# Kernel tuning notes

Measured on AMD Instinct MI355X. Metric: run time of the kernel, lower is better.

## Reference

```python
import jax, jax.numpy as jnp
import numpy as np

EPS = 0.1  # label smoothing

def lstm_scan(x, Wih, Whh, b, reverse=False):
    # x: [B,T,D] -> outputs [B,T,H]; PyTorch gate order i,f,g,o; zero initial state
    B = x.shape[0]; H = Whh.shape[1]
    def cell(carry, xt):
        h, c = carry
        g = xt @ Wih.T + h @ Whh.T + b
        i, f, gg, o = jnp.split(g, 4, axis=-1)
        c2 = jax.nn.sigmoid(f) * c + jax.nn.sigmoid(i) * jnp.tanh(gg)
        h2 = jax.nn.sigmoid(o) * jnp.tanh(c2)
        return (h2, c2), h2
    init = (jnp.zeros((B, H), x.dtype), jnp.zeros((B, H), x.dtype))
    _, hs = jax.lax.scan(cell, init, jnp.swapaxes(x, 0, 1), reverse=reverse)
    return jnp.swapaxes(hs, 0, 1)

def _forward(x, x_mask, y, y_mask,
             enc_l1_Wih, enc_l1_Whh, enc_l1_b, enc_l2_Wih, enc_l2_Whh, enc_l2_b,
             enc_l3_Wih, enc_l3_Whh, enc_l3_b, blstm_f_Wih, blstm_f_Whh, blstm_f_b,
             blstm_b_Wih, blstm_b_Whh, blstm_b_b, conv1_W, conv1_b, conv2_W, conv2_b,
             emb, att_Wih, att_Whh, att_b, w_W, w_b, v_W, v_b, w_att_v,
             dec_Wih, dec_Whh, dec_b, cls_W, cls_b):
    B, T, F0 = x.shape
    pad = (-T) % 4
    # mod_pad + mod_cat: stack 4 consecutive frames -> [B, T//4, 4*F0]
    xp = jnp.pad(x, ((0, 0), (0, pad), (0, 0)))
    xs = xp.reshape(B, (T + pad) // 4, 4 * F0)
    mp = jnp.pad(x_mask, ((0, 0), (0, pad), (0, 0)))
    m = mp[:, ::4, :]  # [B, T', 1]
    # ---- Encoder ----
    h = lstm_scan(xs, enc_l1_Wih, enc_l1_Whh, enc_l1_b)
    h = lstm_scan(h, enc_l2_Wih, enc_l2_Whh, enc_l2_b)
    h = lstm_scan(h, enc_l3_Wih, enc_l3_Whh, enc_l3_b) * m
    bf = lstm_scan(h, blstm_f_Wih, blstm_f_Whh, blstm_f_b)
    bb = lstm_scan(h, blstm_b_Wih, blstm_b_Whh, blstm_b_b, reverse=True)
    bl = jnp.concatenate([bf, bb], axis=-1) * m  # [B,T',1024]
    c1 = jax.nn.leaky_relu(bl @ conv1_W.T + conv1_b, negative_slope=0.1)  # dropout = eval identity
    eout = (c1 @ conv2_W.T + conv2_b) * m  # [B,T',256]
    # ---- Decoder (attention loop via scan) ----
    att_h = eout @ w_W.T + w_b  # [B,T',256]
    embed = emb[y[:, :-1]]      # [B,L-1,256]
    mask_add = (m[:, :, 0] - 1.0) * 1e30  # [B,T']
    P = att_Whh.shape[1]
    h0 = jnp.zeros((B, P), eout.dtype)
    carry0 = (h0, h0, jnp.zeros((B, P), eout.dtype))
    def step(carry, e_t):
        hh, cc, ctx = carry
        body = jnp.concatenate([e_t, ctx], axis=-1)
        g = body @ att_Wih.T + hh @ att_Whh.T + att_b
        i, f, gg, o = jnp.split(g, 4, axis=-1)
        cc = jax.nn.sigmoid(f) * cc + jax.nn.sigmoid(i) * jnp.tanh(gg)
        hh = jax.nn.sigmoid(o) * jnp.tanh(cc)
        state = hh @ v_W.T + v_b  # [B,256]
        score = jnp.sum(w_att_v * jnp.tanh(state[:, None, :] + att_h), axis=-1) + mask_add
        alpha = jax.nn.softmax(score, axis=1)  # [B,T']
        ctx = jnp.sum(eout * alpha[:, :, None], axis=1)  # [B,256]
        return (hh, cc, ctx), (hh, ctx)
    _, (lstms, ctxs) = jax.lax.scan(step, carry0, jnp.swapaxes(embed, 0, 1))
    lstms = jnp.swapaxes(lstms, 0, 1)  # [B,L-1,256]
    ctxs = jnp.swapaxes(ctxs, 0, 1)
    ym = y_mask[:, 1:, None]
    att_fea = jnp.concatenate([lstms * ym, ctxs * ym], axis=-1)  # [B,L-1,512]
    dout = lstm_scan(att_fea, dec_Wih, dec_Whh, dec_b)
    dout = jnp.concatenate([att_fea, dout], axis=-1) * ym  # [B,L-1,768]; dropout = eval identity
    logit = dout @ cls_W.T + cls_b  # [B,L-1,V]
    # ---- Label smoothing CE over real tokens ----
    V = cls_b.shape[0]
    logp = jax.nn.log_softmax(logit, axis=-1)
    label = y[:, 1:]
    mask = (y_mask[:, 1:] > 0).astype(logit.dtype)
    n = jnp.sum(mask)
    smooth = jnp.sum(-jnp.sum(logp, axis=-1) * mask) / n
    nll = jnp.sum(-jnp.take_along_axis(logp, label[:, :, None], axis=-1)[:, :, 0] * mask) / n
    return smooth * EPS / V + (1.0 - EPS) * nll

def setup_inputs() -> dict:
    B, T, F0, L, V = 32, 4096, 80, 65, 4235
    H, P = 512, 256
    key = jax.random.key(0)
    ks = iter(jax.random.split(key, 64))
    def rn(shape, s=0.05):
        return (jax.random.normal(next(ks), shape, jnp.float32) * s)
    inp = {}
    inp['x'] = jax.random.normal(next(ks), (B, T, F0), jnp.float32)
    inp['x_mask'] = jnp.ones((B, T, 1), jnp.float32)
    inp['y'] = jax.random.randint(next(ks), (B, L), 0, V)
    inp['y_mask'] = jnp.ones((B, L), jnp.float32)
    Din = 4 * F0
    inp['enc_l1_Wih'] = rn((4 * H, Din)); inp['enc_l1_Whh'] = rn((4 * H, H)); inp['enc_l1_b'] = jnp.zeros((4 * H,), jnp.float32)
    inp['enc_l2_Wih'] = rn((4 * H, H)); inp['enc_l2_Whh'] = rn((4 * H, H)); inp['enc_l2_b'] = jnp.zeros((4 * H,), jnp.float32)
    inp['enc_l3_Wih'] = rn((4 * H, H)); inp['enc_l3_Whh'] = rn((4 * H, H)); inp['enc_l3_b'] = jnp.zeros((4 * H,), jnp.float32)
    inp['blstm_f_Wih'] = rn((4 * H, H)); inp['blstm_f_Whh'] = rn((4 * H, H)); inp['blstm_f_b'] = jnp.zeros((4 * H,), jnp.float32)
    inp['blstm_b_Wih'] = rn((4 * H, H)); inp['blstm_b_Whh'] = rn((4 * H, H)); inp['blstm_b_b'] = jnp.zeros((4 * H,), jnp.float32)
    inp['conv1_W'] = rn((H, 2 * H)); inp['conv1_b'] = jnp.zeros((H,), jnp.float32)
    inp['conv2_W'] = rn((P, H)); inp['conv2_b'] = jnp.zeros((P,), jnp.float32)
    inp['emb'] = rn((V, P), 1.0)
    inp['att_Wih'] = rn((4 * P, 2 * P)); inp['att_Whh'] = rn((4 * P, P)); inp['att_b'] = jnp.zeros((4 * P,), jnp.float32)
    inp['w_W'] = rn((P, P)); inp['w_b'] = jnp.zeros((P,), jnp.float32)
    inp['v_W'] = rn((P, P)); inp['v_b'] = jnp.zeros((P,), jnp.float32)
    inp['w_att_v'] = rn((P,))
    inp['dec_Wih'] = rn((4 * P, 2 * P)); inp['dec_Whh'] = rn((4 * P, P)); inp['dec_b'] = jnp.zeros((4 * P,), jnp.float32)
    inp['cls_W'] = rn((V, 3 * P)); inp['cls_b'] = jnp.zeros((V,), jnp.float32)
    return inp

def reference(x, x_mask, y, y_mask, enc_l1_Wih, enc_l1_Whh, enc_l1_b, enc_l2_Wih, enc_l2_Whh, enc_l2_b, enc_l3_Wih, enc_l3_Whh, enc_l3_b, blstm_f_Wih, blstm_f_Whh, blstm_f_b, blstm_b_Wih, blstm_b_Whh, blstm_b_b, conv1_W, conv1_b, conv2_W, conv2_b, emb, att_Wih, att_Whh, att_b, w_W, w_b, v_W, v_b, w_att_v, dec_Wih, dec_Whh, dec_b, cls_W, cls_b):
    return _forward(x, x_mask, y, y_mask, enc_l1_Wih, enc_l1_Whh, enc_l1_b, enc_l2_Wih, enc_l2_Whh, enc_l2_b, enc_l3_Wih, enc_l3_Whh, enc_l3_b, blstm_f_Wih, blstm_f_Whh, blstm_f_b, blstm_b_Wih, blstm_b_Whh, blstm_b_b, conv1_W, conv1_b, conv2_W, conv2_b, emb, att_Wih, att_Whh, att_b, w_W, w_b, v_W, v_b, w_att_v, dec_Wih, dec_Whh, dec_b, cls_W, cls_b)
```

## Files before the change

kernel.cpp:

```cpp
#include <hip/hip_runtime.h>
#include <math.h>

#define DEV static __device__ __forceinline__
typedef unsigned short u16;
typedef unsigned int u32;

typedef __attribute__((ext_vector_type(8))) __bf16 bf16x8;
typedef __attribute__((ext_vector_type(4))) float f32x4;

DEV float sigm(float x){ return 1.0f/(1.0f+__expf(-x)); }
DEV float tanh_f(float x){ float e=__expf(2.0f*x); return 1.0f - 2.0f/(e+1.0f); }

DEV float b2f(u16 u){ union {u32 i; float f;} c; c.i = ((u32)u)<<16; return c.f; }
DEV u16 f2b(float f){ union {u32 i; float f;} c; c.f = f; u32 r = (c.i + 0x7FFFu + ((c.i>>16)&1u)) >> 16; return (u16)r; }

DEV void cstore(u32* p, u32 v){ __hip_atomic_store(p, v, __ATOMIC_RELAXED, __HIP_MEMORY_SCOPE_SYSTEM); }
DEV u32  cload(const u32* p){ return __hip_atomic_load(p, __ATOMIC_RELAXED, __HIP_MEMORY_SCOPE_SYSTEM); }

#define FSTRIDE 32
DEV void waitflags(unsigned* flags, unsigned target, int nwg){
  const int lane = threadIdx.x & 63;
  unsigned long long spin = 0;
  for(;;){
    bool ok = true;
    for (int j=lane; j<nwg; j+=64)
      ok &= ((int)(cload(&flags[j*FSTRIDE]) - target) >= 0);
    if (__all(ok)) break;
    if (++spin > 2000000ull) break;
    __builtin_amdgcn_s_sleep(1);
  }
}

struct PL2 { const float *Wih, *Whh, *bias; const u16* xplain; u16* hout; int kx, maskout; };
struct PA2 {
  PL2 L[4];
  u16* ex;
  u16* exm;
  const float* xm;
  unsigned* flags;
  int T, nwg, rev; unsigned base;
};

#define VWAIT(N) { asm volatile("s_waitcnt vmcnt(" #N ")" ::: "memory"); __builtin_amdgcn_sched_barrier(0); }

#define STAGE_LO(LL, Q, TT) { \
  const char* base_; int coh_; \
  if ((LL)==0){ base_=(const char*)A.L[0].xplain + ((long)(TT)*32768) + w*512; coh_=0; } \
  else if (NL==4 && (LL)==3){ base_=(const char*)A.exm + (long)par*32768 + w*512; coh_=1; } \
  else { base_=(const char*)A.ex + (long)(((LL)-1)*2+par)*32768 + w*512; coh_=1; } \
  _Pragma("unroll") \
  for (int i_=0;i_<8;++i_){ \
    int rl_=i_*2+(lane>>5); \
    int b_=bh*16+rl_; \
    const char* src_=base_ + (long)b_*1024 + (((lane&31)*16) ^ ((rl_&7)<<4)); \
    char* dst_=Vs + (Q)*32768 + w*8192 + i_*1024 + lane*16; \
    if (coh_) __builtin_amdgcn_global_load_lds((const u32*)src_,(u32*)dst_,16,0,0x11); \
    else      __builtin_amdgcn_global_load_lds((const u32*)src_,(u32*)dst_,16,0,0); \
  } }

#define STAGE_HI(LL, Q) { \
  const char* base_=(const char*)A.ex + (long)((LL)*2+par)*32768 + (w-2)*512; \
  _Pragma("unroll") \
  for (int i_=0;i_<8;++i_){ \
    int rl_=i_*2+(lane>>5); \
    int b_=bh*16+rl_; \
    const char* src_=base_ + (long)b_*1024 + (((lane&31)*16) ^ ((rl_&7)<<4)); \
    char* dst_=Vs + (Q)*32768 + w*8192 + i_*1024 + lane*16; \
    __builtin_amdgcn_global_load_lds((const u32*)src_,(u32*)dst_,16,0,0x11); \
  } }

#define STAGE_ALL(LL, Q, TT) { if (w<2) STAGE_LO(LL, Q, TT) else STAGE_HI(LL, Q) }

#define DOMFMA(LL, Q) { \
  const char* vb_=Vs + (Q)*32768 + w*8192; \
  const int sw_=(cl&7)<<4; \
  f32x4 a0_={0.f,0.f,0.f,0.f}, a1_={0.f,0.f,0.f,0.f}; \
  _Pragma("unroll") \
  for (int f_=0;f_<8;++f_){ \
    union{ bf16x8 v; uint4 q; } aa_; \
    aa_.q = *(const uint4*)(vb_ + cl*512 + ((f_*64+lg*16) ^ sw_)); \
    a0_=__builtin_amdgcn_mfma_f32_16x16x32_bf16(aa_.v, bw[LL][0][f_], a0_,0,0,0); \
    a1_=__builtin_amdgcn_mfma_f32_16x16x32_bf16(aa_.v, bw[LL][1][f_], a1_,0,0,0); \
  } \
  *(f32x4*)&P[(LL)*2560 + (w*32 + cl)*20 + lg*4] = a0_; \
  *(f32x4*)&P[(LL)*2560 + (w*32 + 16 + cl)*20 + lg*4] = a1_; \
  __builtin_amdgcn_sched_barrier(0); }

template<int NL>
__global__ __launch_bounds__(256,1) void pipe2(PA2 A){
  __shared__ __align__(16) char Vs[98304];
  __shared__ float P[NL*2560];
  const int t = threadIdx.x, wg = blockIdx.x;
  const int bh = wg>>6, cg = wg&63;
  const int w = t>>6, lane = t&63;
  const int cl = lane&15, lg = lane>>4;
  u32* exu  = (u32*)A.ex;
  u32* exmu = (u32*)A.exm;
  bf16x8 bw[NL][2][8];
  #pragma unroll
  for (int l=0;l<NL;++l){
    const int kx = A.L[l].kx;
    #pragma unroll
    for (int nt=0; nt<2; ++nt){
      const int c32 = nt*16 + cl;
      const int r = (c32&3)*512 + cg*8 + (c32>>2);
      #pragma unroll
      for (int f=0;f<8;++f){
        union { bf16x8 v; u16 s[8]; } u;
        int k8 = w*256 + f*32 + lg*8;
        if (k8 < 512){
          if (k8 < kx){
            const float* p = A.L[l].Wih + (long)r*kx + k8;
            for (int j=0;j<8;++j) u.s[j]=f2b(p[j]);
          } else { for (int j=0;j<8;++j) u.s[j]=0; }
        } else {
          const float* p = A.L[l].Whh + (long)r*512 + (k8-512);
          for (int j=0;j<8;++j) u.s[j]=f2b(p[j]);
        }
        bw[l][nt][f]=u.v;
      }
    }
  }
  float bias_r[NL][4];
  float cst_r[NL];
  #pragma unroll
  for (int l=0;l<NL;++l) cst_r[l]=0.f;
  if (t<128){
    const int uu = t>>4;
    #pragma unroll
    for (int l=0;l<NL;++l)
      #pragma unroll
      for (int g=0;g<4;++g)
        bias_r[l][g] = A.L[l].bias[g*512 + cg*8 + uu];
  }
  {
    const int tot = (NL==4)? 640 : 128;
    for (int i=t;i<tot;i+=256){
      int l5=i>>7, rem=i&127;
      int par0=rem>>6, bl=(rem>>2)&15, j=rem&3;
      int b=bh*16+bl;
      u32* p = (l5<NL)? exu + (l5*2+par0)*8192 + b*256 + cg*4 + j
                      : exmu + par0*8192 + b*256 + cg*4 + j;
      cstore(p,0);
    }
  }
  __syncthreads();
  if (t==0) cstore(&A.flags[wg*FSTRIDE], A.base+1);
  const int T = A.T;
  unsigned* myflags = A.flags + (bh*64)*FSTRIDE;
  for (int s=0; s<T+NL-1; ++s){
    const int par = (s-1)&1;
    if constexpr (NL==1){
      const int tt0 = A.rev ? (T-1-s) : s;
      if (w<2) STAGE_LO(0,0,tt0)
      waitflags(myflags, A.base+s+1, 64);
      if (w>=2) STAGE_HI(0,0)
      VWAIT(0)
      DOMFMA(0,0)
    } else {
      if (s>=3 && s<=T-1){
        const int tt0 = A.rev ? (T-1-s) : s;
        if (w<2) STAGE_LO(0,0,tt0)
        waitflags(myflags, A.base+s+1, 64);
        if (w>=2) STAGE_HI(0,0)
        STAGE_ALL(1,1,0)
        STAGE_ALL(2,2,0)
        VWAIT(16) DOMFMA(0,0)
        asm volatile("s_waitcnt lgkmcnt(0)" ::: "memory");
        __builtin_amdgcn_sched_barrier(0);
        STAGE_ALL(3,0,0)
        VWAIT(16) DOMFMA(1,1)
        VWAIT(8)  DOMFMA(2,2)
        VWAIT(0)  DOMFMA(3,0)
      } else {
        waitflags(myflags, A.base+s+1, 64);
        #pragma unroll
        for (int l=0;l<NL;++l){
          const int sc = s-l;
          if (sc<0 || sc>=T) continue;
          const int ttl = A.rev ? (T-1-sc) : sc;
          STAGE_ALL(l, (l&1), ttl)
          VWAIT(0)
          DOMFMA(l, (l&1))
        }
      }
    }
    __syncthreads();
    if (t<128){
      const int bl = t&15, uu = t>>4;
      const int b = bh*16 + bl;
      #pragma unroll
      for (int l=0;l<NL;++l){
        const int sc = s-l;
        if (sc<0 || sc>=T) continue;
        const int tt = A.rev ? (T-1-sc) : sc;
        float g4[4];
        #pragma unroll
        for (int g=0;g<4;++g){
          const int c32 = uu*4+g;
          float sum = bias_r[l][g];
          #pragma unroll
          for (int ww=0;ww<4;++ww) sum += P[l*2560 + (ww*32+c32)*20 + bl];
          g4[g]=sum;
        }
        float c2 = sigm(g4[1])*cst_r[l] + sigm(g4[0])*tanh_f(g4[2]);
        float h2 = sigm(g4[3])*tanh_f(c2);
        cst_r[l]=c2;
        float h2n = __shfl_down(h2, 16);
        if (!(uu&1)){
          u32 pk = (u32)f2b(h2) | ((u32)f2b(h2n)<<16);
          cstore(exu + (l*2+(s&1))*8192 + b*256 + cg*4 + (uu>>1), pk);
        }
        if (NL==4 && l==2){
          float m = A.xm[b*4096 + 4*tt];
          float hm = h2*m;
          float hmn = __shfl_down(hm, 16);
          if (!(uu&1)){
            u32 pk = (u32)f2b(hm) | ((u32)f2b(hmn)<<16);
            cstore(exmu + (s&1)*8192 + b*256 + cg*4 + (uu>>1), pk);
          }
          if (A.L[2].hout) A.L[2].hout[((long)tt*32+b)*512 + cg*8+uu] = f2b(hm);
        } else if (A.L[l].hout){
          float ov = h2;
          if (A.L[l].maskout) ov *= A.xm[b*4096 + 4*tt];
          A.L[l].hout[((long)tt*32+b)*512 + cg*8+uu] = f2b(ov);
        }
      }
    }
    __syncthreads();
    if (t==0) cstore(&A.flags[wg*FSTRIDE], A.base+s+2);
  }
}

__global__ __launch_bounds__(256,1) void dec_rec2(
    const u16* __restrict__ xin, const float* __restrict__ Wih,
    const float* __restrict__ Whh, const float* __restrict__ bias,
    float* __restrict__ dout, u16* __restrict__ exd,
    unsigned* flags, unsigned base, int T)
{
  __shared__ __align__(16) char Vs[49152];
  __shared__ float P[2304];
  __shared__ float cst[128];
  __shared__ float biasl[16];
  const int t = threadIdx.x, wg = blockIdx.x;
  const int u0 = wg*4;
  const int w = t>>6, lane = t&63, c = lane&15, lg = lane>>4;
  const int r = (c&3)*256 + u0 + (c>>2);
  u32* exu = (u32*)exd;
  const int nf = (w<2) ? 8 : 4;
  bf16x8 bw[8];
  #pragma unroll
  for (int f=0;f<8;++f){
    union { bf16x8 v; u16 s[8]; } u;
    if (f < nf){
      if (w<2){
        const float* p = Wih + (long)r*512 + w*256 + f*32 + lg*8;
        for (int j=0;j<8;++j) u.s[j]=f2b(p[j]);
      } else {
        const float* p = Whh + (long)r*256 + (w-2)*128 + f*32 + lg*8;
        for (int j=0;j<8;++j) u.s[j]=f2b(p[j]);
      }
    } else { for (int j=0;j<8;++j) u.s[j]=0; }
    bw[f]=u.v;
  }
  if (t<16) biasl[t] = bias[(t&3)*256 + u0 + (t>>2)];
  if (t<128) cst[t]=0.f;
  if (t<128){
    int par=(t>>6)&1, b=(t>>1)&31, j=t&1;
    cstore(exu + par*4096 + b*128 + wg*2 + j, 0);
  }
  __syncthreads();
  if (t==0) cstore(&flags[wg*FSTRIDE], base+1);
  const int waveOff = (w<2) ? w*16384 : 32768 + (w-2)*8192;
  const int NI  = (w<2) ? 16 : 8;
  const int rpi = (w<2) ? 2 : 4;
  const int sb  = (w<2) ? (lane>>5) : (lane>>4);
  const int coffb = (w<2) ? (lane&31)*16 : (lane&15)*16;
  const int rowB = (w<2) ? 512 : 256;
  for (int s=0; s<T; ++s){
    if (w<2){
      #pragma unroll
      for (int i=0;i<16;++i){
        int b = i*rpi + sb;
        const char* src = (const char*)xin + (long)s*32768 + w*512 + b*1024 + (coffb ^ ((b&7)<<4));
        void* ldst = (void*)(Vs + waveOff + i*1024);
        __builtin_amdgcn_global_load_lds((const u32*)src, (u32*)ldst, 16, 0, 0);
      }
    }
    waitflags(flags, base+s+1, 64);
    const int par = (s-1)&1;
    if (w>=2){
      #pragma unroll
      for (int i=0;i<8;++i){
        int b = i*rpi + sb;
        const char* src = (const char*)exd + par*16384 + (w-2)*256 + b*512 + (coffb ^ ((b&7)<<4));
        void* ldst = (void*)(Vs + waveOff + i*1024);
        __builtin_amdgcn_global_load_lds((const u32*)src, (u32*)ldst, 16, 0, 0x11);
      }
    }
    asm volatile("s_waitcnt vmcnt(0)" ::: "memory");
    __builtin_amdgcn_sched_barrier(0);
    f32x4 acc0={0.f,0.f,0.f,0.f}, acc1={0.f,0.f,0.f,0.f};
    const int b1 = c+16;
    #pragma unroll
    for (int f=0;f<8;++f){
      if (f>=nf) break;
      int koff = f*64 + lg*16;
      union { bf16x8 v; uint4 q; } a0, a1;
      a0.q = *(const uint4*)(Vs + waveOff + c *rowB + (koff ^ ((c &7)<<4)));
      a1.q = *(const uint4*)(Vs + waveOff + b1*rowB + (koff ^ ((b1&7)<<4)));
      acc0 = __builtin_amdgcn_mfma_f32_16x16x32_bf16(a0.v, bw[f], acc0, 0,0,0);
      acc1 = __builtin_amdgcn_mfma_f32_16x16x32_bf16(a1.v, bw[f], acc1, 0,0,0);
    }
    {
      float* pp = &P[(w*16+c)*36 + lg*4];
      *(f32x4*)pp      = acc0;
      *(f32x4*)(pp+16) = acc1;
    }
    __syncthreads();
    if (t<128){
      const int b = t&31, uu = t>>5, wpw = t>>6;
      float g4[4];
      #pragma unroll
      for (int g=0; g<4; ++g){
        int cc = uu*4+g;
        float sum = biasl[cc];
        #pragma unroll
        for (int ww=0; ww<4; ++ww) sum += P[(ww*16+cc)*36 + b];
        g4[g]=sum;
      }
      float c2 = sigm(g4[1])*cst[t] + sigm(g4[0])*tanh_f(g4[2]);
      float h2 = sigm(g4[3])*tanh_f(c2);
      cst[t]=c2;
      u32 hv = (u32)f2b(h2);
      u32 ot = (u32)__shfl_xor((int)hv, 32);
      if (lane<32)
        cstore(exu + (s&1)*4096 + b*128 + wg*2 + wpw, (hv&0xffffu)|(ot<<16));
      dout[((long)s*32+b)*256 + u0+uu] = h2;
    }
    __syncthreads();
    if (t==0) cstore(&flags[wg*FSTRIDE], base+s+2);
  }
}

__global__ void cvt_x(const float* __restrict__ x, u16* __restrict__ xp){
  long id8 = ((long)blockIdx.x*256 + threadIdx.x)*8;
  int rr = (int)(id8 >> 9); int k = (int)(id8 & 511);
  int tt = rr >> 5, b = rr & 31;
  union { uint4 q; u16 s[8]; } u;
  if (k < 320){
    const float* p = x + (long)b*327680 + (long)tt*320 + k;
    float4 v0 = *(const float4*)p, v1 = *(const float4*)(p+4);
    u.s[0]=f2b(v0.x); u.s[1]=f2b(v0.y); u.s[2]=f2b(v0.z); u.s[3]=f2b(v0.w);
    u.s[4]=f2b(v1.x); u.s[5]=f2b(v1.y); u.s[6]=f2b(v1.z); u.s[7]=f2b(v1.w);
  } else {
    for (int j=0;j<8;++j) u.s[j]=0;
  }
  *(uint4*)(xp + id8) = u.q;
}

template<int ABF, int CBF>
__global__ __launch_bounds__(256,2) void gemm_mfma(
  const void* __restrict__ A0, long lda0, const void* __restrict__ A1, long lda1, int K0,
  const float* __restrict__ W, const float* __restrict__ bias, void* __restrict__ C,
  int M, int N, int K, int ldw, int act, const float* __restrict__ xmask)
{
  __shared__ __align__(16) u16 As[64*32];
  __shared__ __align__(16) u16 Bs[64*32];
  const int t = threadIdx.x;
  const int m0 = blockIdx.x*64, n0 = blockIdx.y*64;
  const int w = t>>6, lane = t&63;
  const int al = lane&15, lg = lane>>4;
  f32x4 acc[4];
  #pragma unroll
  for (int i=0;i<4;++i) acc[i] = (f32x4){0.f,0.f,0.f,0.f};
  const int srow = t>>2, kq = t&3;
  const int spos = (kq ^ (srow&3))*8;
  for (int k0=0; k0<K; k0+=32){
    {
      int kk = k0 + kq*8;
      const void* Ab; long lda; int kof;
      if (kk < K0){ Ab=A0; lda=lda0; kof=kk; } else { Ab=A1; lda=lda1; kof=kk-K0; }
      union { uint4 q; u16 s[8]; } u;
      if (ABF){
        u.q = *(const uint4*)((const u16*)Ab + (long)(m0+srow)*lda + kof);
      } else {
        const float* ap = (const float*)Ab + (long)(m0+srow)*lda + kof;
        float4 x0 = *(const float4*)ap, x1 = *(const float4*)(ap+4);
        u.s[0]=f2b(x0.x); u.s[1]=f2b(x0.y); u.s[2]=f2b(x0.z); u.s[3]=f2b(x0.w);
        u.s[4]=f2b(x1.x); u.s[5]=f2b(x1.y); u.s[6]=f2b(x1.z); u.s[7]=f2b(x1.w);
      }
      *(uint4*)&As[srow*32 + spos] = u.q;
    }
    {
      int n = n0 + srow;
      union { uint4 q; u16 s[8]; } u;
      if (n < N){
        const float* wp = W + (long)n*ldw + k0 + kq*8;
        float4 y0 = *(const float4*)wp, y1 = *(const float4*)(wp+4);
        u.s[0]=f2b(y0.x); u.s[1]=f2b(y0.y); u.s[2]=f2b(y0.z); u.s[3]=f2b(y0.w);
        u.s[4]=f2b(y1.x); u.s[5]=f2b(y1.y); u.s[6]=f2b(y1.z); u.s[7]=f2b(y1.w);
      } else {
        for (int j=0;j<8;++j) u.s[j]=0;
      }
      *(uint4*)&Bs[srow*32 + spos] = u.q;
    }
    __syncthreads();
    union { bf16x8 v; uint4 q; } a;
    a.q = *(const uint4*)&As[(w*16+al)*32 + ((lg ^ (al&3))*8)];
    #pragma unroll
    for (int nt=0; nt<4; ++nt){
      union { bf16x8 v; uint4 q; } b;
      b.q = *(const uint4*)&Bs[(nt*16+al)*32 + ((lg ^ (al&3))*8)];
      acc[nt] = __builtin_amdgcn_mfma_f32_16x16x32_bf16(a.v, b.v, acc[nt], 0,0,0);
    }
    __syncthreads();
  }
  #pragma unroll
  for (int nt=0; nt<4; ++nt){
    int n = n0 + nt*16 + al;
    if (n >= N) continue;
    float bv = bias[n];
    #pragma unroll
    for (int j=0;j<4;++j){
      int m = m0 + w*16 + lg*4 + j;
      float v = acc[nt][j] + bv;
      if (act) v = (v > 0.f) ? v : 0.1f*v;
      if (xmask) v *= xmask[(m&31)*4096 + 4*(m>>5)];
      if (CBF) ((u16*)C)[(long)m*N + n] = f2b(v);
      else     ((float*)C)[(long)m*N + n] = v;
    }
  }
}

__global__ void embed_gather(const float* __restrict__ emb, const int* __restrict__ y,
                             float* __restrict__ out){
  int id = blockIdx.x*256 + threadIdx.x;
  int p = id&255, r = id>>8;
  int l = r>>5, b = r&31;
  out[id] = emb[(long)y[b*65 + l]*256 + p];
}

__global__ void zero_f(float* __restrict__ p, int n){
  int id = blockIdx.x*256 + threadIdx.x;
  if (id < n) p[id] = 0.f;
}

__global__ void set_val(float* p, float v){ p[0] = v; }

__global__ void attfea_k(const float* __restrict__ lstms, const float* __restrict__ ctxs,
                         const float* __restrict__ ym, float* __restrict__ attf,
                         u16* __restrict__ attfb){
  long id4 = ((long)blockIdx.x*256 + threadIdx.x)*4;
  int r = (int)(id4>>9); int f = (int)(id4&511);
  int l = r>>5, b = r&31;
  float m = ym[b*65 + l + 1];
  float4 v = (f<256) ? *(const float4*)(lstms + (long)r*256 + f)
                     : *(const float4*)(ctxs  + (long)r*256 + (f-256));
  v.x*=m; v.y*=m; v.z*=m; v.w*=m;
  *(float4*)(attf + id4) = v;
  u16* ob = attfb + id4;
  ob[0]=f2b(v.x); ob[1]=f2b(v.y); ob[2]=f2b(v.z); ob[3]=f2b(v.w);
}

__global__ void dcat_k(const float* __restrict__ attf, const float* __restrict__ dout,
                       const float* __restrict__ ym, float* __restrict__ dcat){
  long id4 = ((long)blockIdx.x*256 + threadIdx.x)*4;
  int r = (int)(id4/768); int f = (int)(id4 - (long)r*768);
  int l = r>>5, b = r&31;
  float m = ym[b*65 + l + 1];
  float4 v = (f<512) ? *(const float4*)(attf + (long)r*512 + f)
                     : *(const float4*)(dout + (long)r*256 + (f-512));
  v.x*=m; v.y*=m; v.z*=m; v.w*=m;
  *(float4*)(dcat + id4) = v;
}

__global__ __launch_bounds__(256,1) void k1_dec(
  const float* __restrict__ bodyR, float* __restrict__ bodyW,
  const float* __restrict__ epart, const float* __restrict__ Whh,
  const float* __restrict__ Wih, float* __restrict__ cc,
  float* __restrict__ lstms, int s)
{
  __shared__ __align__(16) float vT[512*36];
  __shared__ float gl[32*32];
  const int t = threadIdx.x, wg = blockIdx.x;
  for (int i = t*4; i < 32*512; i += 1024){
    int b = i>>9, k = i&511;
    float4 v = *(const float4*)(bodyR + b*512 + k);
    vT[(k+0)*36+b]=v.x; vT[(k+1)*36+b]=v.y; vT[(k+2)*36+b]=v.z; vT[(k+3)*36+b]=v.w;
  }
  __syncthreads();
  const int c_l = t>>3, bq = t&7;
  const int col = (c_l&3)*256 + wg*8 + (c_l>>2);
  float a0=0.f,a1=0.f,a2=0.f,a3=0.f;
  for (int k=0;k<256;k+=4){
    float4 w = *(const float4*)(Whh + (long)col*256 + k);
    const float* vp = &vT[k*36 + bq*4];
    float4 v0=*(const float4*)(vp), v1=*(const float4*)(vp+36), v2=*(const float4*)(vp+72), v3=*(const float4*)(vp+108);
    a0 += w.x*v0.x + w.y*v1.x + w.z*v2.x + w.w*v3.x;
    a1 += w.x*v0.y + w.y*v1.y + w.z*v2.y + w.w*v3.y;
    a2 += w.x*v0.z + w.y*v1.z + w.z*v2.z + w.w*v3.z;
    a3 += w.x*v0.w + w.y*v1.w + w.z*v2.w + w.w*v3.w;
  }
  for (int k=256;k<512;k+=4){
    float4 w = *(const float4*)(Wih + (long)col*512 + k);
    const float* vp = &vT[k*36 + bq*4];
    float4 v0=*(const float4*)(vp), v1=*(const float4*)(vp+36), v2=*(const float4*)(vp+72), v3=*(const float4*)(vp+108);
    a0 += w.x*v0.x + w.y*v1.x + w.z*v2.x + w.w*v3.x;
    a1 += w.x*v0.y + w.y*v1.y + w.z*v2.y + w.w*v3.y;
    a2 += w.x*v0.z + w.y*v1.z + w.z*v2.z + w.w*v3.z;
    a3 += w.x*v0.w + w.y*v1.w + w.z*v2.w + w.w*v3.w;
  }
  gl[c_l*32+bq*4+0] = a0 + epart[((long)s*32 + bq*4+0)*1024 + col];
  gl[c_l*32+bq*4+1] = a1 + epart[((long)s*32 + bq*4+1)*1024 + col];
  gl[c_l*32+bq*4+2] = a2 + epart[((long)s*32 + bq*4+2)*1024 + col];
  gl[c_l*32+bq*4+3] = a3 + epart[((long)s*32 + bq*4+3)*1024 + col];
  __syncthreads();
  {
    const int u_ = t>>5, b = t&31, ug = wg*8 + u_;
    const float gi=gl[(u_*4+0)*32+b], gf=gl[(u_*4+1)*32+b], gg=gl[(u_*4+2)*32+b], go=gl[(u_*4+3)*32+b];
    float c0 = cc[b*256+ug];
    float c2 = sigm(gf)*c0 + sigm(gi)*tanh_f(gg);
    float h2 = sigm(go)*tanh_f(c2);
    cc[b*256+ug] = c2;
    bodyW[b*512 + ug] = h2;
    lstms[((long)s*32 + b)*256 + ug] = h2;
  }
}

__global__ __launch_bounds__(256,1) void k2_dec(
  const float* __restrict__ bodyW, const float* __restrict__ vW,
  const float* __restrict__ vb, float* __restrict__ state)
{
  __shared__ __align__(16) float hT[256*36];
  const int t = threadIdx.x, wg = blockIdx.x;
  for (int i = t*4; i < 8192; i += 1024){
    int b = i>>8, k = i&255;
    float4 v = *(const float4*)(bodyW + b*512 + k);
    hT[(k+0)*36+b]=v.x; hT[(k+1)*36+b]=v.y; hT[(k+2)*36+b]=v.z; hT[(k+3)*36+b]=v.w;
  }
  __syncthreads();
  const int p = wg*32 + (t>>3), bq = t&7;
  float a0=0.f,a1=0.f,a2=0.f,a3=0.f;
  for (int k=0;k<256;k+=4){
    float4 w = *(const float4*)(vW + (long)p*256 + k);
    const float* vp = &hT[k*36 + bq*4];
    float4 v0=*(const float4*)(vp), v1=*(const float4*)(vp+36), v2=*(const float4*)(vp+72), v3=*(const float4*)(vp+108);
    a0 += w.x*v0.x + w.y*v1.x + w.z*v2.x + w.w*v3.x;
    a1 += w.x*v0.y + w.y*v1.y + w.z*v2.y + w.w*v3.y;
    a2 += w.x*v0.z + w.y*v1.z + w.z*v2.z + w.w*v3.z;
    a3 += w.x*v0.w + w.y*v1.w + w.z*v2.w + w.w*v3.w;
  }
  float bb = vb[p];
  state[(bq*4+0)*256 + p] = a0 + bb;
  state[(bq*4+1)*256 + p] = a1 + bb;
  state[(bq*4+2)*256 + p] = a2 + bb;
  state[(bq*4+3)*256 + p] = a3 + bb;
}

__global__ __launch_bounds__(256,1) void k3_dec(
  const float* __restrict__ state, const u16* __restrict__ atth,
  const float* __restrict__ wav, const float* __restrict__ xm,
  float* __restrict__ sc, float* __restrict__ scm)
{
  __shared__ float st[256], wv[256], red[256];
  const int t = threadIdx.x;
  const int b = blockIdx.x>>2, ch = blockIdx.x&3;
  st[t] = state[b*256 + t];
  wv[t] = wav[t];
  __syncthreads();
  const int tp = ch*256 + t;
  const u16* ap = atth + ((long)tp*32 + b)*256;
  float acc = 0.f;
  for (int p=0;p<256;p+=4){
    ushort4 a = *(const ushort4*)(ap+p);
    acc += wv[p+0]*tanh_f(st[p+0]+b2f(a.x));
    acc += wv[p+1]*tanh_f(st[p+1]+b2f(a.y));
    acc += wv[p+2]*tanh_f(st[p+2]+b2f(a.z));
    acc += wv[p+3]*tanh_f(st[p+3]+b2f(a.w));
  }
  acc += (xm[b*4096 + 4*tp] - 1.0f)*1e30f;
  sc[b*1024 + tp] = acc;
  red[t] = acc;
  __syncthreads();
  for (int o=128;o>0;o>>=1){ if (t<o) red[t]=fmaxf(red[t],red[t+o]); __syncthreads(); }
  if (t==0) scm[b*4+ch] = red[0];
}

__global__ __launch_bounds__(256,1) void k4_dec(
  const float* __restrict__ sc, const float* __restrict__ scm,
  const u16* __restrict__ eout, float* __restrict__ ctxs,
  float* __restrict__ bodyW, int s)
{
  __shared__ float al[1024];
  __shared__ float red[256];
  const int t = threadIdx.x, b = blockIdx.x;
  float m = fmaxf(fmaxf(scm[b*4+0],scm[b*4+1]), fmaxf(scm[b*4+2],scm[b*4+3]));
  float ps = 0.f;
  #pragma unroll
  for (int j=0;j<4;++j){
    int tp = t + j*256;
    float e = __expf(sc[b*1024+tp] - m);
    al[tp] = e; ps += e;
  }
  red[t]=ps; __syncthreads();
  for (int o=128;o>0;o>>=1){ if (t<o) red[t]+=red[t+o]; __syncthreads(); }
  float rinv = 1.0f/red[0];
  float acc = 0.f;
  const u16* ep = eout + b*256 + t;
  for (int tp=0;tp<1024;++tp) acc += al[tp] * b2f(ep[(long)tp*8192]);
  float cv = acc*rinv;
  ctxs[((long)s*32 + b)*256 + t] = cv;
  bodyW[b*512 + 256 + t] = cv;
}

__global__ __launch_bounds__(256,1) void loss_row(
  const float* __restrict__ logits, const int* __restrict__ y,
  const float* __restrict__ ym, float* __restrict__ rows)
{
  __shared__ float red[256];
  const int r = blockIdx.x, t = threadIdx.x;
  const float* row = logits + (long)r*4235;
  float mx = -3.0e38f;
  for (int i=t;i<4235;i+=256) mx = fmaxf(mx, row[i]);
  red[t]=mx; __syncthreads();
  for (int o=128;o>0;o>>=1){ if (t<o) red[t]=fmaxf(red[t],red[t+o]); __syncthreads(); }
  const float M = red[0];
  __syncthreads();
  float se=0.f, sl=0.f;
  for (int i=t;i<4235;i+=256){ float v=row[i]; se += __expf(v-M); sl += v; }
  red[t]=se; __syncthreads();
  for (int o=128;o>0;o>>=1){ if (t<o) red[t]+=red[t+o]; __syncthreads(); }
  const float SE = red[0];
  __syncthreads();
  red[t]=sl; __syncthreads();
  for (int o=128;o>0;o>>=1){ if (t<o) red[t]+=red[t+o]; __syncthreads(); }
  const float SL = red[0];
  if (t==0){
    const int tt = r>>5, b = r&31;
    const float lse = M + logf(SE);
    const float mk = (ym[b*65 + tt + 1] > 0.f) ? 1.f : 0.f;
    rows[r]        = (4235.0f*lse - SL)*mk;
    rows[2048 + r] = (lse - row[y[b*65 + tt + 1]])*mk;
    rows[4096 + r] = mk;
  }
}

__global__ __launch_bounds__(256,1) void loss_final(const float* __restrict__ rows, float* __restrict__ out){
  __shared__ float red[256];
  const int t = threadIdx.x;
  float s1=0.f,s2=0.f,s3=0.f;
  for (int i=t;i<2048;i+=256){ s1+=rows[i]; s2+=rows[2048+i]; s3+=rows[4096+i]; }
  red[t]=s1; __syncthreads();
  for (int o=128;o>0;o>>=1){ if (t<o) red[t]+=red[t+o]; __syncthreads(); }
  const float S = red[0]; __syncthreads();
  red[t]=s2; __syncthreads();
  for (int o=128;o>0;o>>=1){ if (t<o) red[t]+=red[t+o]; __syncthreads(); }
  const float NL = red[0]; __syncthreads();
  red[t]=s3; __syncthreads();
  for (int o=128;o>0;o>>=1){ if (t<o) red[t]+=red[t+o]; __syncthreads(); }
  const float N = red[0];
  if (t==0){
    float n = (N > 0.f) ? N : 1.f;
    out[0] = (S/n)*(0.1f/4235.0f) + 0.9f*(NL/n);
  }
}

extern "C" void kernel_launch(void* const* d_in, const int* in_sizes, int n_in,
                              void* d_out, int out_size, void* d_ws, size_t ws_size,
                              hipStream_t stream)
{
  const float* x    = (const float*)d_in[0];
  const float* xm   = (const float*)d_in[1];
  const int*   y    = (const int*)  d_in[2];
  const float* ym   = (const float*)d_in[3];
  const float* l1_Wih=(const float*)d_in[4];  const float* l1_Whh=(const float*)d_in[5];  const float* l1_b=(const float*)d_in[6];
  const float* l2_Wih=(const float*)d_in[7];  const float* l2_Whh=(const float*)d_in[8];  const float* l2_b=(const float*)d_in[9];
  const float* l3_Wih=(const float*)d_in[10]; const float* l3_Whh=(const float*)d_in[11]; const float* l3_b=(const float*)d_in[12];
  const float* bf_Wih=(const float*)d_in[13]; const float* bf_Whh=(const float*)d_in[14]; const float* bf_b=(const float*)d_in[15];
  const float* bb_Wih=(const float*)d_in[16]; const float* bb_Whh=(const float*)d_in[17]; const float* bb_b=(const float*)d_in[18];
  const float* c1_W=(const float*)d_in[19]; const float* c1_b=(const float*)d_in[20];
  const float* c2_W=(const float*)d_in[21]; const float* c2_b=(const float*)d_in[22];
  const float* emb =(const float*)d_in[23];
  const float* att_Wih=(const float*)d_in[24]; const float* att_Whh=(const float*)d_in[25]; const float* att_b=(const float*)d_in[26];
  const float* w_W=(const float*)d_in[27]; const float* w_b=(const float*)d_in[28];
  const float* v_W=(const float*)d_in[29]; const float* v_b=(const float*)d_in[30];
  const float* wav=(const float*)d_in[31];
  const float* dec_Wih=(const float*)d_in[32]; const float* dec_Whh=(const float*)d_in[33]; const float* dec_b=(const float*)d_in[34];
  const float* cls_W=(const float*)d_in[35]; const float* cls_b=(const float*)d_in[36];

  const size_t REQ = 137625600ull;
  if (ws_size < REQ){
    set_val<<<1,1,0,stream>>>((float*)d_out, -(float)(ws_size>>20));
    return;
  }
  char* ws = (char*)d_ws;
  unsigned* FLAGS  = (unsigned*)(ws);
  unsigned* FLAGSD = (unsigned*)(ws + 16384);
  u16* EXU  = (u16*)(ws + 65536);
  u16* EXM  = (u16*)(ws + 327680);
  u16* EXD  = (u16*)(ws + 393216);
  u16* XP   = (u16*)(ws + 2097152);
  u16* HS2  = (u16*)(ws + 35651584);
  u16* HSF  = (u16*)(ws + 69206016);
  u16* HSB  = XP;
  u16* C1OUT = HS2;
  u16* EOUTB = HSF;
  u16* ATTHB = (u16*)(ws + 85983232);
  float* LOGIT = (float*)XP;
  float* AR    = (float*)(ws + 102760448);
  float* EMBED = AR;
  float* EPART = EMBED + 524288;
  float* LSTMS = EPART + 2097152;
  float* CTXS  = LSTMS + 524288;
  float* ATTF  = CTXS  + 524288;
  float* DOUT  = ATTF  + 1048576;
  float* DCAT  = DOUT  + 524288;
  float* SC    = DCAT  + 1572864;
  float* SCM   = SC    + 32768;
  float* ROWS  = SCM   + 128;
  float* BODY  = ROWS  + 6144;
  float* CC    = BODY  + 32768;
  float* STATE = CC    + 8192;
  u16*  ATTFB  = (u16*)(STATE + 8192);

  (void)hipMemsetAsync(ws, 0, 32768, stream);

  cvt_x<<<8192,256,0,stream>>>(x, XP);
  PA2 pa;
  pa.L[0] = { l1_Wih, l1_Whh, l1_b, XP,      nullptr, 320, 0 };
  pa.L[1] = { l2_Wih, l2_Whh, l2_b, nullptr, nullptr, 512, 0 };
  pa.L[2] = { l3_Wih, l3_Whh, l3_b, nullptr, HS2,     512, 0 };
  pa.L[3] = { bf_Wih, bf_Whh, bf_b, nullptr, HSF,     512, 1 };
  pa.ex = EXU; pa.exm = EXM; pa.xm = xm; pa.flags = FLAGS;
  pa.T = 1024; pa.nwg = 128; pa.rev = 0; pa.base = 0;
  pipe2<4><<<128,256,0,stream>>>(pa);
  PA2 pb;
  pb.L[0] = { bb_Wih, bb_Whh, bb_b, HS2, HSB, 512, 1 };
  pb.L[1] = pb.L[0]; pb.L[2] = pb.L[0]; pb.L[3] = pb.L[0];
  pb.ex = EXU; pb.exm = EXM; pb.xm = xm; pb.flags = FLAGS;
  pb.T = 1024; pb.nwg = 128; pb.rev = 1; pb.base = 1028;
  pipe2<1><<<128,256,0,stream>>>(pb);
  gemm_mfma<1,1><<<dim3(512,8),256,0,stream>>>(HSF, 512, HSB, 512, 512,
      c1_W, c1_b, C1OUT, 32768, 512, 1024, 1024, 1, nullptr);
  gemm_mfma<1,1><<<dim3(512,4),256,0,stream>>>(C1OUT, 512, C1OUT, 512, 512,
      c2_W, c2_b, EOUTB, 32768, 256, 512, 512, 0, xm);
  gemm_mfma<1,1><<<dim3(512,4),256,0,stream>>>(EOUTB, 256, EOUTB, 256, 256,
      w_W, w_b, ATTHB, 32768, 256, 256, 256, 0, nullptr);

  embed_gather<<<2048,256,0,stream>>>(emb, y, EMBED);
  gemm_mfma<0,0><<<dim3(32,16),256,0,stream>>>(EMBED, 256, EMBED, 256, 256,
      att_Wih, att_b, EPART, 2048, 1024, 256, 512, 0, nullptr);
  zero_f<<<160,256,0,stream>>>(BODY, 40960);
  for (int s=0;s<64;++s){
    float* bodyR = BODY + (s&1)*16384;
    float* bodyW = BODY + ((s+1)&1)*16384;
    k1_dec<<<32,256,0,stream>>>(bodyR, bodyW, EPART, att_Whh, att_Wih, CC, LSTMS, s);
    k2_dec<<<8,256,0,stream>>>(bodyW, v_W, v_b, STATE);
    k3_dec<<<128,256,0,stream>>>(STATE, ATTHB, wav, xm, SC, SCM);
    k4_dec<<<32,256,0,stream>>>(SC, SCM, EOUTB, CTXS, bodyW, s);
  }
  attfea_k<<<1024,256,0,stream>>>(LSTMS, CTXS, ym, ATTF, ATTFB);
  dec_rec2<<<64,256,0,stream>>>(ATTFB, dec_Wih, dec_Whh, dec_b,
      DOUT, EXD, FLAGSD, 0u, 64);
  dcat_k<<<1536,256,0,stream>>>(ATTF, DOUT, ym, DCAT);
  gemm_mfma<0,0><<<dim3(32,67),256,0,stream>>>(DCAT, 768, DCAT, 768, 768,
      cls_W, cls_b, LOGIT, 2048, 4235, 768, 768, 0, nullptr);
  loss_row<<<2048,256,0,stream>>>(LOGIT, y, ym, ROWS);
  loss_final<<<1,256,0,stream>>>(ROWS, (float*)d_out);
}
```

Before: 18.23 ms.

## Fuse attention decoder loop into one persistent kernel with flag barriers

Replaces the 256 small per-step kernel launches of the attention decoder (k1..k4 for each of 64 steps) with a single persistent 128-workgroup kernel. Grid-wide spin-flag barriers separate the LSTM, state-projection/score and softmax-context phases. The v_W projection is now computed redundantly per workgroup instead of in a separate kernel. This removes launch overhead and inter-kernel gaps, but adds system-scope atomic loads/stores, spin-wait cost, and reliance on all 128 workgroups being co-resident.

```diff
diff --git a/kernel.cpp b/kernel.cpp
--- a/kernel.cpp
+++ b/kernel.cpp
@@ -16,6 +16,8 @@
 
 DEV void cstore(u32* p, u32 v){ __hip_atomic_store(p, v, __ATOMIC_RELAXED, __HIP_MEMORY_SCOPE_SYSTEM); }
 DEV u32  cload(const u32* p){ return __hip_atomic_load(p, __ATOMIC_RELAXED, __HIP_MEMORY_SCOPE_SYSTEM); }
+DEV float cloadf(const float* p){ union{u32 i;float f;}c; c.i = cload((const u32*)p); return c.f; }
+DEV void cstoref(float* p, float v){ union{u32 i;float f;}c; c.f = v; cstore((u32*)p, c.i); }
 
 #define FSTRIDE 32
 DEV void waitflags(unsigned* flags, unsigned target, int nwg){
@@ -343,6 +345,144 @@
   }
 }
 
+__global__ __launch_bounds__(256,1) void dec_att(
+  const float* __restrict__ epart, const float* __restrict__ Whh,
+  const float* __restrict__ Wih, const float* __restrict__ vW,
+  const float* __restrict__ vb, const float* __restrict__ wav,
+  const u16* __restrict__ atth, const u16* __restrict__ eout,
+  const float* __restrict__ xm,
+  float* __restrict__ body, float* __restrict__ cc,
+  float* __restrict__ lstms, float* __restrict__ ctxs,
+  float* __restrict__ sc, float* __restrict__ scm,
+  unsigned* __restrict__ flags)
+{
+  __shared__ __align__(16) char LDSB[77824];
+  const int t = threadIdx.x, wg = blockIdx.x;
+  if (wg < 64) cstoref(body + wg*256 + t, 0.f);
+  if (wg < 32) cc[((t&31))*256 + wg*8 + (t>>5)] = 0.f;
+  __syncthreads();
+  if (t==0) cstore(&flags[wg*FSTRIDE], 1);
+  waitflags(flags, 1, 128);
+  for (int s=0; s<64; ++s){
+    float* bodyR = body + (s&1)*16384;
+    float* bodyW = body + ((s+1)&1)*16384;
+    if (wg < 32){
+      float* vT = (float*)LDSB;
+      float* gl = (float*)(LDSB + 73728);
+      for (int i = t*4; i < 32*512; i += 1024){
+        int b = i>>9, k = i&511;
+        float v0 = cloadf(bodyR + b*512 + k);
+        float v1 = cloadf(bodyR + b*512 + k+1);
+        float v2 = cloadf(bodyR + b*512 + k+2);
+        float v3 = cloadf(bodyR + b*512 + k+3);
+        vT[(k+0)*36+b]=v0; vT[(k+1)*36+b]=v1; vT[(k+2)*36+b]=v2; vT[(k+3)*36+b]=v3;
+      }
+      __syncthreads();
+      const int c_l = t>>3, bq = t&7;
+      const int col = (c_l&3)*256 + wg*8 + (c_l>>2);
+      float a0=0.f,a1=0.f,a2=0.f,a3=0.f;
+      for (int k=0;k<256;k+=4){
+        float4 w = *(const float4*)(Whh + (long)col*256 + k);
+        const float* vp = &vT[k*36 + bq*4];
+        float4 v0=*(const float4*)(vp), v1=*(const float4*)(vp+36), v2=*(const float4*)(vp+72), v3=*(const float4*)(vp+108);
+        a0 += w.x*v0.x + w.y*v1.x + w.z*v2.x + w.w*v3.x;
+        a1 += w.x*v0.y + w.y*v1.y + w.z*v2.y + w.w*v3.y;
+        a2 += w.x*v0.z + w.y*v1.z + w.z*v2.z + w.w*v3.z;
+        a3 += w.x*v0.w + w.y*v1.w + w.z*v2.w + w.w*v3.w;
+      }
+      for (int k=256;k<512;k+=4){
+        float4 w = *(const float4*)(Wih + (long)col*512 + k);
+        const float* vp = &vT[k*36 + bq*4];
+        float4 v0=*(const float4*)(vp), v1=*(const float4*)(vp+36), v2=*(const float4*)(vp+72), v3=*(const float4*)(vp+108);
+        a0 += w.x*v0.x + w.y*v1.x + w.z*v2.x + w.w*v3.x;
+        a1 += w.x*v0.y + w.y*v1.y + w.z*v2.y + w.w*v3.y;
+        a2 += w.x*v0.z + w.y*v1.z + w.z*v2.z + w.w*v3.z;
+        a3 += w.x*v0.w + w.y*v1.w + w.z*v2.w + w.w*v3.w;
+      }
+      gl[c_l*32+bq*4+0] = a0 + epart[((long)s*32 + bq*4+0)*1024 + col];
+      gl[c_l*32+bq*4+1] = a1 + epart[((long)s*32 + bq*4+1)*1024 + col];
+      gl[c_l*32+bq*4+2] = a2 + epart[((long)s*32 + bq*4+2)*1024 + col];
+      gl[c_l*32+bq*4+3] = a3 + epart[((long)s*32 + bq*4+3)*1024 + col];
+      __syncthreads();
+      {
+        const int u_ = t>>5, b = t&31, ug = wg*8 + u_;
+        const float gi=gl[(u_*4+0)*32+b], gf=gl[(u_*4+1)*32+b], gg=gl[(u_*4+2)*32+b], go=gl[(u_*4+3)*32+b];
+        float c0 = cc[b*256+ug];
+        float c2 = sigm(gf)*c0 + sigm(gi)*tanh_f(gg);
+        float h2 = sigm(go)*tanh_f(c2);
+        cc[b*256+ug] = c2;
+        cstoref(bodyW + b*512 + ug, h2);
+        lstms[((long)s*32 + b)*256 + ug] = h2;
+      }
+    }
+    __syncthreads();
+    if (t==0) cstore(&flags[wg*FSTRIDE], s*3+2);
+    waitflags(flags, s*3+2, 128);
+    {
+      const int b = wg>>2, ch = wg&3;
+      float* hh = (float*)LDSB;
+      float* st = (float*)(LDSB+1024);
+      float* wv = (float*)(LDSB+2048);
+      float* red= (float*)(LDSB+3072);
+      hh[t] = cloadf(bodyW + b*512 + t);
+      wv[t] = wav[t];
+      __syncthreads();
+      float a = vb[t];
+      for (int k=0;k<256;k+=4){
+        float4 w = *(const float4*)(vW + (long)t*256 + k);
+        a += w.x*hh[k] + w.y*hh[k+1] + w.z*hh[k+2] + w.w*hh[k+3];
+      }
+      st[t] = a;
+      __syncthreads();
+      const int tp = ch*256 + t;
+      const u16* ap = atth + ((long)tp*32 + b)*256;
+      float acc = 0.f;
+      for (int p=0;p<256;p+=4){
+        ushort4 av = *(const ushort4*)(ap+p);
+        acc += wv[p+0]*tanh_f(st[p+0]+b2f(av.x));
+        acc += wv[p+1]*tanh_f(st[p+1]+b2f(av.y));
+        acc += wv[p+2]*tanh_f(st[p+2]+b2f(av.z));
+        acc += wv[p+3]*tanh_f(st[p+3]+b2f(av.w));
+      }
+      acc += (xm[b*4096 + 4*tp] - 1.0f)*1e30f;
+      cstoref(sc + b*1024 + tp, acc);
+      red[t] = acc;
+      __syncthreads();
+      for (int o=128;o>0;o>>=1){ if (t<o) red[t]=fmaxf(red[t],red[t+o]); __syncthreads(); }
+      if (t==0) cstoref(scm + b*4+ch, red[0]);
+    }
+    __syncthreads();
+    if (t==0) cstore(&flags[wg*FSTRIDE], s*3+3);
+    waitflags(flags, s*3+3, 128);
+    if (wg < 32){
+      const int b = wg;
+      float* al = (float*)LDSB;
+      float* red= (float*)(LDSB+4096);
+      float m = fmaxf(fmaxf(cloadf(scm+b*4+0),cloadf(scm+b*4+1)),
+                      fmaxf(cloadf(scm+b*4+2),cloadf(scm+b*4+3)));
+      float ps = 0.f;
+      #pragma unroll
+      for (int j=0;j<4;++j){
+        int tp = t + j*256;
+        float e = __expf(cloadf(sc + b*1024+tp) - m);
+        al[tp] = e; ps += e;
+      }
+      red[t]=ps; __syncthreads();
+      for (int o=128;o>0;o>>=1){ if (t<o) red[t]+=red[t+o]; __syncthreads(); }
+      float rinv = 1.0f/red[0];
+      float acc = 0.f;
+      const u16* ep = eout + b*256 + t;
+      for (int tp=0;tp<1024;++tp) acc += al[tp] * b2f(ep[(long)tp*8192]);
+      float cv = acc*rinv;
+      ctxs[((long)s*32 + b)*256 + t] = cv;
+      cstoref(bodyW + b*512 + 256 + t, cv);
+    }
+    __syncthreads();
+    if (t==0) cstore(&flags[wg*FSTRIDE], s*3+4);
+    waitflags(flags, s*3+4, 128);
+  }
+}
+
 __global__ void cvt_x(const float* __restrict__ x, u16* __restrict__ xp){
   long id8 = ((long)blockIdx.x*256 + threadIdx.x)*8;
   int rr = (int)(id8 >> 9); int k = (int)(id8 & 511);
@@ -441,11 +581,6 @@
   out[id] = emb[(long)y[b*65 + l]*256 + p];
 }
 
-__global__ void zero_f(float* __restrict__ p, int n){
-  int id = blockIdx.x*256 + threadIdx.x;
-  if (id < n) p[id] = 0.f;
-}
-
 __global__ void set_val(float* p, float v){ p[0] = v; }
 
 __global__ void attfea_k(const float* __restrict__ lstms, const float* __restrict__ ctxs,
@@ -473,145 +608,6 @@
                      : *(const float4*)(dout + (long)r*256 + (f-512));
   v.x*=m; v.y*=m; v.z*=m; v.w*=m;
   *(float4*)(dcat + id4) = v;
-}
-
-__global__ __launch_bounds__(256,1) void k1_dec(
-  const float* __restrict__ bodyR, float* __restrict__ bodyW,
-  const float* __restrict__ epart, const float* __restrict__ Whh,
-  const float* __restrict__ Wih, float* __restrict__ cc,
-  float* __restrict__ lstms, int s)
-{
-  __shared__ __align__(16) float vT[512*36];
-  __shared__ float gl[32*32];
-  const int t = threadIdx.x, wg = blockIdx.x;
-  for (int i = t*4; i < 32*512; i += 1024){
-    int b = i>>9, k = i&511;
-    float4 v = *(const float4*)(bodyR + b*512 + k);
-    vT[(k+0)*36+b]=v.x; vT[(k+1)*36+b]=v.y; vT[(k+2)*36+b]=v.z; vT[(k+3)*36+b]=v.w;
-  }
-  __syncthreads();
-  const int c_l = t>>3, bq = t&7;
-  const int col = (c_l&3)*256 + wg*8 + (c_l>>2);
-  float a0=0.f,a1=0.f,a2=0.f,a3=0.f;
-  for (int k=0;k<256;k+=4){
-    float4 w = *(const float4*)(Whh + (long)col*256 + k);
-    const float* vp = &vT[k*36 + bq*4];
-    float4 v0=*(const float4*)(vp), v1=*(const float4*)(vp+36), v2=*(const float4*)(vp+72), v3=*(const float4*)(vp+108);
-    a0 += w.x*v0.x + w.y*v1.x + w.z*v2.x + w.w*v3.x;
-    a1 += w.x*v0.y + w.y*v1.y + w.z*v2.y + w.w*v3.y;
-    a2 += w.x*v0.z + w.y*v1.z + w.z*v2.z + w.w*v3.z;
-    a3 += w.x*v0.w + w.y*v1.w + w.z*v2.w + w.w*v3.w;
-  }
-  for (int k=256;k<512;k+=4){
-    float4 w = *(const float4*)(Wih + (long)col*512 + k);
-    const float* vp = &vT[k*36 + bq*4];
-    float4 v0=*(const float4*)(vp), v1=*(const float4*)(vp+36), v2=*(const float4*)(vp+72), v3=*(const float4*)(vp+108);
-    a0 += w.x*v0.x + w.y*v1.x + w.z*v2.x + w.w*v3.x;
-    a1 += w.x*v0.y + w.y*v1.y + w.z*v2.y + w.w*v3.y;
-    a2 += w.x*v0.z + w.y*v1.z + w.z*v2.z + w.w*v3.z;
-    a3 += w.x*v0.w + w.y*v1.w + w.z*v2.w + w.w*v3.w;
-  }
-  gl[c_l*32+bq*4+0] = a0 + epart[((long)s*32 + bq*4+0)*1024 + col];
-  gl[c_l*32+bq*4+1] = a1 + epart[((long)s*32 + bq*4+1)*1024 + col];
-  gl[c_l*32+bq*4+2] = a2 + epart[((long)s*32 + bq*4+2)*1024 + col];
-  gl[c_l*32+bq*4+3] = a3 + epart[((long)s*32 + bq*4+3)*1024 + col];
-  __syncthreads();
-  {
-    const int u_ = t>>5, b = t&31, ug = wg*8 + u_;
-    const float gi=gl[(u_*4+0)*32+b], gf=gl[(u_*4+1)*32+b], gg=gl[(u_*4+2)*32+b], go=gl[(u_*4+3)*32+b];
-    float c0 = cc[b*256+ug];
-    float c2 = sigm(gf)*c0 + sigm(gi)*tanh_f(gg);
-    float h2 = sigm(go)*tanh_f(c2);
-    cc[b*256+ug] = c2;
-    bodyW[b*512 + ug] = h2;
-    lstms[((long)s*32 + b)*256 + ug] = h2;
-  }
-}
-
-__global__ __launch_bounds__(256,1) void k2_dec(
-  const float* __restrict__ bodyW, const float* __restrict__ vW,
-  const float* __restrict__ vb, float* __restrict__ state)
-{
-  __shared__ __align__(16) float hT[256*36];
-  const int t = threadIdx.x, wg = blockIdx.x;
-  for (int i = t*4; i < 8192; i += 1024){
-    int b = i>>8, k = i&255;
-    float4 v = *(const float4*)(bodyW + b*512 + k);
-    hT[(k+0)*36+b]=v.x; hT[(k+1)*36+b]=v.y; hT[(k+2)*36+b]=v.z; hT[(k+3)*36+b]=v.w;
-  }
-  __syncthreads();
-  const int p = wg*32 + (t>>3), bq = t&7;
-  float a0=0.f,a1=0.f,a2=0.f,a3=0.f;
-  for (int k=0;k<256;k+=4){
-    float4 w = *(const float4*)(vW + (long)p*256 + k);
-    const float* vp = &hT[k*36 + bq*4];
-    float4 v0=*(const float4*)(vp), v1=*(const float4*)(vp+36), v2=*(const float4*)(vp+72), v3=*(const float4*)(vp+108);
-    a0 += w.x*v0.x + w.y*v1.x + w.z*v2.x + w.w*v3.x;
-    a1 += w.x*v0.y + w.y*v1.y + w.z*v2.y + w.w*v3.y;
-    a2 += w.x*v0.z + w.y*v1.z + w.z*v2.z + w.w*v3.z;
-    a3 += w.x*v0.w + w.y*v1.w + w.z*v2.w + w.w*v3.w;
-  }
-  float bb = vb[p];
-  state[(bq*4+0)*256 + p] = a0 + bb;
-  state[(bq*4+1)*256 + p] = a1 + bb;
-  state[(bq*4+2)*256 + p] = a2 + bb;
-  state[(bq*4+3)*256 + p] = a3 + bb;
-}
-
-__global__ __launch_bounds__(256,1) void k3_dec(
-  const float* __restrict__ state, const u16* __restrict__ atth,
-  const float* __restrict__ wav, const float* __restrict__ xm,
-  float* __restrict__ sc, float* __restrict__ scm)
-{
-  __shared__ float st[256], wv[256], red[256];
-  const int t = threadIdx.x;
-  const int b = blockIdx.x>>2, ch = blockIdx.x&3;
-  st[t] = state[b*256 + t];
-  wv[t] = wav[t];
-  __syncthreads();
-  const int tp = ch*256 + t;
-  const u16* ap = atth + ((long)tp*32 + b)*256;
-  float acc = 0.f;
-  for (int p=0;p<256;p+=4){
-    ushort4 a = *(const ushort4*)(ap+p);
-    acc += wv[p+0]*tanh_f(st[p+0]+b2f(a.x));
-    acc += wv[p+1]*tanh_f(st[p+1]+b2f(a.y));
-    acc += wv[p+2]*tanh_f(st[p+2]+b2f(a.z));
-    acc += wv[p+3]*tanh_f(st[p+3]+b2f(a.w));
-  }
-  acc += (xm[b*4096 + 4*tp] - 1.0f)*1e30f;
-  sc[b*1024 + tp] = acc;
-  red[t] = acc;
-  __syncthreads();
-  for (int o=128;o>0;o>>=1){ if (t<o) red[t]=fmaxf(red[t],red[t+o]); __syncthreads(); }
-  if (t==0) scm[b*4+ch] = red[0];
-}
-
-__global__ __launch_bounds__(256,1) void k4_dec(
-  const float* __restrict__ sc, const float* __restrict__ scm,
-  const u16* __restrict__ eout, float* __restrict__ ctxs,
-  float* __restrict__ bodyW, int s)
-{
-  __shared__ float al[1024];
-  __shared__ float red[256];
-  const int t = threadIdx.x, b = blockIdx.x;
-  float m = fmaxf(fmaxf(scm[b*4+0],scm[b*4+1]), fmaxf(scm[b*4+2],scm[b*4+3]));
-  float ps = 0.f;
-  #pragma unroll
-  for (int j=0;j<4;++j){
-    int tp = t + j*256;
-    float e = __expf(sc[b*1024+tp] - m);
-    al[tp] = e; ps += e;
-  }
-  red[t]=ps; __syncthreads();
-  for (int o=128;o>0;o>>=1){ if (t<o) red[t]+=red[t+o]; __syncthreads(); }
-  float rinv = 1.0f/red[0];
-  float acc = 0.f;
-  const u16* ep = eout + b*256 + t;
-  for (int tp=0;tp<1024;++tp) acc += al[tp] * b2f(ep[(long)tp*8192]);
-  float cv = acc*rinv;
-  ctxs[((long)s*32 + b)*256 + t] = cv;
-  bodyW[b*512 + 256 + t] = cv;
 }
 
 __global__ __launch_bounds__(256,1) void loss_row(
@@ -721,10 +717,9 @@
   float* ROWS  = SCM   + 128;
   float* BODY  = ROWS  + 6144;
   float* CC    = BODY  + 32768;
-  float* STATE = CC    + 8192;
-  u16*  ATTFB  = (u16*)(STATE + 8192);
-
-  (void)hipMemsetAsync(ws, 0, 32768, stream);
+  u16*  ATTFB  = (u16*)(CC + 8192);
+
+  (void)hipMemsetAsync(ws, 0, 65536, stream);
 
   cvt_x<<<8192,256,0,stream>>>(x, XP);
   PA2 pa;
@@ -751,18 +746,11 @@
   embed_gather<<<2048,256,0,stream>>>(emb, y, EMBED);
   gemm_mfma<0,0><<<dim3(32,16),256,0,stream>>>(EMBED, 256, EMBED, 256, 256,
       att_Wih, att_b, EPART, 2048, 1024, 256, 512, 0, nullptr);
-  zero_f<<<160,256,0,stream>>>(BODY, 40960);
-  for (int s=0;s<64;++s){
-    float* bodyR = BODY + (s&1)*16384;
-    float* bodyW = BODY + ((s+1)&1)*16384;
-    k1_dec<<<32,256,0,stream>>>(bodyR, bodyW, EPART, att_Whh, att_Wih, CC, LSTMS, s);
-    k2_dec<<<8,256,0,stream>>>(bodyW, v_W, v_b, STATE);
-    k3_dec<<<128,256,0,stream>>>(STATE, ATTHB, wav, xm, SC, SCM);
-    k4_dec<<<32,256,0,stream>>>(SC, SCM, EOUTB, CTXS, bodyW, s);
-  }
+  dec_att<<<128,256,0,stream>>>(EPART, att_Whh, att_Wih, v_W, v_b, wav,
+      ATTHB, EOUTB, xm, BODY, CC, LSTMS, CTXS, SC, SCM, FLAGSD);
   attfea_k<<<1024,256,0,stream>>>(LSTMS, CTXS, ym, ATTF, ATTFB);
   dec_rec2<<<64,256,0,stream>>>(ATTFB, dec_Wih, dec_Whh, dec_b,
-      DOUT, EXD, FLAGSD, 0u, 64);
+      DOUT, EXD, FLAGSD, 193u, 64);
   dcat_k<<<1536,256,0,stream>>>(ATTF, DOUT, ym, DCAT);
   gemm_mfma<0,0><<<dim3(32,67),256,0,stream>>>(DCAT, 768, DCAT, 768, 768,
       cls_W, cls_b, LOGIT, 2048, 4235, 768, 768, 0, nullptr);
```

Result: slower. 27.66 ms (+51.7%).
